# Kernel optimization log

Hardware: AMD Instinct MI355X
Metric: run time of the kernel (lower is better)

## Reference

```python
import jax, jax.numpy as jnp
import numpy as np

NUM_HEADS = 8
LN_EPS = 1e-5


def _pos_enc(h, w, dim, dtype):
    # PositionalEncodingPermute2D: channels = ceil(dim/2)
    ch = int(np.ceil(dim / 2))
    inv = jnp.asarray(1.0 / (10000.0 ** (np.arange(0, ch, 2, dtype=np.float32) / ch)))
    px = jnp.arange(h, dtype=jnp.float32)[:, None] * inv  # (h, ch//2)
    py = jnp.arange(w, dtype=jnp.float32)[:, None] * inv  # (w, ch//2)
    ex = jnp.concatenate([jnp.sin(px), jnp.cos(px)], -1)  # (h, ch)
    ey = jnp.concatenate([jnp.sin(py), jnp.cos(py)], -1)  # (w, ch)
    emb = jnp.concatenate([
        jnp.broadcast_to(ex[:, None, :], (h, w, ch)),
        jnp.broadcast_to(ey[None, :, :], (h, w, ch)),
    ], -1)[:, :, :dim]  # (h, w, dim)
    return emb.transpose(2, 0, 1).astype(dtype)  # (dim, h, w)


def _pool(x, s):
    # AdaptiveAvgPool2d(s) with h, w divisible by s
    b, c, h, w = x.shape
    return x.reshape(b, c, s, h // s, s, w // s).mean((3, 5))


def _dsc(y, dw_w, pw_w):
    # depthwise 3x3 (groups=C, pad 1, no bias) + pointwise 1x1 (no bias)
    dn = ('NCHW', 'OIHW', 'NCHW')
    y = jax.lax.conv_general_dilated(y, dw_w, (1, 1), 'SAME',
                                     feature_group_count=y.shape[1],
                                     dimension_numbers=dn)
    return jax.lax.conv_general_dilated(y, pw_w, (1, 1), 'SAME',
                                        dimension_numbers=dn)


def setup_inputs() -> dict:
    key = jax.random.key(0)
    ks = jax.random.split(key, 8)
    b, c, h, w = 8, 128, 128, 128
    s = 0.02
    return {
        'x': jax.random.normal(ks[0], (b, c, h, w), jnp.float32),
        'Wq': jax.random.normal(ks[1], (c, c), jnp.float32) * s,
        'Wkv': jax.random.normal(ks[2], (2 * c, c), jnp.float32) * s,
        'Wproj': jax.random.normal(ks[3], (c, c), jnp.float32) * s,
        'bproj': jnp.zeros((c,), jnp.float32),
        'dw_w': jax.random.normal(ks[4], (c, 1, 3, 3), jnp.float32) * np.sqrt(2.0 / 9.0),
        'pw_w': jax.random.normal(ks[5], (c, c, 1, 1), jnp.float32) * np.sqrt(2.0 / c),
        'ln_w': jnp.ones((c,), jnp.float32),
        'ln_b': jnp.zeros((c,), jnp.float32),
    }


def reference(x, Wq, Wkv, Wproj, bproj, dw_w, pw_w, ln_w, ln_b):
    b, c, h, w = x.shape
    m = NUM_HEADS
    hd = c // m
    scale = hd ** -0.5

    xp = x + _pos_enc(h, w, c, x.dtype)[None]        # (b,c,h,w)
    xt = xp.reshape(b, c, h * w).transpose(0, 2, 1)  # (b,hw,c)

    q = (xt @ Wq.T).reshape(b, h * w, m, hd).transpose(0, 2, 1, 3)  # (b,m,hw,hd)

    # four ASPP branches through the shared depthwise-separable conv
    branches = []
    for s in (8, 4, 2, 1):
        y = _dsc(_pool(xp, s), dw_w, pw_w)           # (b,c,s,s)
        branches.append(y.reshape(b, c, s * s).transpose(0, 2, 1))
    z = jnp.concatenate(branches, axis=1)            # (b,85,c)

    mu = z.mean(-1, keepdims=True)
    var = ((z - mu) ** 2).mean(-1, keepdims=True)
    z = (z - mu) / jnp.sqrt(var + LN_EPS) * ln_w + ln_b
    z = jax.nn.gelu(z, approximate=False)

    kvlen = z.shape[1]
    kv = (z @ Wkv.T).reshape(b, kvlen, 2, m, hd).transpose(2, 0, 3, 1, 4)  # (2,b,m,kv,hd)
    k, v = kv[0], kv[1]

    attn = jax.nn.softmax(jnp.einsum('bmqd,bmkd->bmqk', q, k) * scale, axis=-1)
    o = jnp.einsum('bmqk,bmkd->bmqd', attn, v)       # (b,m,hw,hd)
    o = o.transpose(0, 2, 1, 3).reshape(b, h * w, c)
    o = o @ Wproj.T + bproj                          # dropout p=0 (eval) is identity
    return o.transpose(0, 2, 1).reshape(b, c, h, w)
```

## Files before the change

### kernel.cpp

```cpp
#include <hip/hip_runtime.h>
#include <stdint.h>

#define OFF_EX   ((size_t)0)
#define OFF_EY   ((size_t)32768)
#define OFF_EXM  ((size_t)65536)
#define OFF_EYM  ((size_t)67584)
#define OFF_WQB  ((size_t)69632)
#define OFF_WPB  ((size_t)102400)
#define OFF_P8   ((size_t)135168)
#define OFF_KWS  ((size_t)393216)
#define OFF_VWS  ((size_t)589824)

typedef __attribute__((ext_vector_type(4)))  float f32x4;
typedef __attribute__((ext_vector_type(16))) float f32x16;
typedef __attribute__((ext_vector_type(8)))  short s16x8;
typedef __attribute__((ext_vector_type(4)))  unsigned int u32x4;

__device__ __forceinline__ uint16_t f2bf(float f){
  uint32_t u = __builtin_bit_cast(uint32_t, f);
  u += 0x7fffu + ((u >> 16) & 1u);
  return (uint16_t)(u >> 16);
}
__device__ __forceinline__ uint32_t cvtpk(float a, float b){
  uint32_t r;
  asm("v_cvt_pk_bf16_f32 %0, %1, %2" : "=v"(r) : "v"(a), "v"(b));
  return r;
}

__global__ __launch_bounds__(256) void kprep(const float* __restrict__ Wq,
                                             const float* __restrict__ Wproj,
                                             char* __restrict__ ws){
  int idx = blockIdx.x * 256 + threadIdx.x;
  float* EX = (float*)(ws + OFF_EX);
  float* EY = (float*)(ws + OFF_EY);
  float* EXM = (float*)(ws + OFF_EXM);
  float* EYM = (float*)(ws + OFF_EYM);
  uint16_t* WQB = (uint16_t*)(ws + OFF_WQB);
  uint16_t* WPB = (uint16_t*)(ws + OFF_WPB);
  if (idx < 8192){
    int i = idx >> 6, d = idx & 63;
    float inv = powf(10000.0f, -(float)(d & 31) * (1.0f/32.0f));
    float a = (float)i * inv;
    EX[idx] = (d < 32) ? sinf(a) : cosf(a);
  } else if (idx < 16384){
    int e = idx - 8192;
    int c = e >> 7, j = e & 127;
    float inv = powf(10000.0f, -(float)(c & 31) * (1.0f/32.0f));
    float a = (float)j * inv;
    EY[e] = (c < 32) ? sinf(a) : cosf(a);
  } else if (idx < 32768){
    int e = idx - 16384;
    WQB[e] = f2bf(Wq[e]);
  } else if (idx < 49152){
    int e = idx - 32768;
    WPB[e] = f2bf(Wproj[e]);
  } else if (idx < 49664){
    int e = idx - 49152; int r8 = e >> 6, c = e & 63;
    float inv = powf(10000.0f, -(float)(c & 31) * (1.0f/32.0f));
    float s = 0.f;
    for (int u = 0; u < 16; ++u){
      float a = (float)(r8*16 + u) * inv;
      s += (c < 32) ? sinf(a) : cosf(a);
    }
    EXM[e] = s * (1.0f/16.0f);
  } else if (idx < 50176){
    int e = idx - 49664; int c8 = e >> 6, c2 = e & 63;
    float inv = powf(10000.0f, -(float)(c2 & 31) * (1.0f/32.0f));
    float s = 0.f;
    for (int w = 0; w < 16; ++w){
      float a = (float)(c8*16 + w) * inv;
      s += (c2 < 32) ? sinf(a) : cosf(a);
    }
    EYM[e] = s * (1.0f/16.0f);
  }
}

__global__ __launch_bounds__(256) void kpool2(const float* __restrict__ x,
                                              char* __restrict__ ws){
  float* P8 = (float*)(ws + OFF_P8);
  int bx = blockIdx.x;
  int b = bx >> 7, c = bx & 127;
  int t = threadIdx.x, lane = t & 63, wv = t >> 6;
  const float* plane = x + ((size_t)(b*128 + c))*16384;
  float acc[8];
  #pragma unroll
  for (int r = 0; r < 8; ++r) acc[r] = 0.f;
  #pragma unroll
  for (int k = 0; k < 16; ++k){
    f32x4 v = *(const f32x4*)(plane + k*1024 + t*4);
    acc[k >> 1] += (v.x + v.y) + (v.z + v.w);
  }
  __shared__ float wred[4][64];
  int bc = (lane >> 2) & 7;
  #pragma unroll
  for (int br = 0; br < 8; ++br){
    float v = acc[br];
    v += __shfl_xor(v, 1);
    v += __shfl_xor(v, 2);
    v += __shfl_xor(v, 32);
    if ((lane & 3) == 0 && lane < 32) wred[wv][br*8 + bc] = v;
  }
  __syncthreads();
  if (t < 64){
    float s = wred[0][t] + wred[1][t] + wred[2][t] + wred[3][t];
    P8[((size_t)(b*128) + c)*64 + t] = s * (1.0f/256.0f);
  }
}

__global__ __launch_bounds__(256) void kaspp(const float* __restrict__ dww,
                                             const float* __restrict__ pww,
                                             const float* __restrict__ Wkv,
                                             const float* __restrict__ lnw,
                                             const float* __restrict__ lnb,
                                             char* __restrict__ ws){
  const float* P8  = (const float*)(ws + OFF_P8);
  const float* EXM = (const float*)(ws + OFF_EXM);
  const float* EYM = (const float*)(ws + OFF_EYM);
  uint16_t* KWS = (uint16_t*)(ws + OFF_KWS);
  uint16_t* VWS = (uint16_t*)(ws + OFF_VWS);
  int bx = blockIdx.x;
  int b = bx / 96;
  int pos = bx % 96;
  int t = threadIdx.x;

  if (pos >= 85){
    if (t < 128){
      int m = t >> 4, hd = t & 15;
      KWS[(((size_t)b*8 + m)*96 + pos)*16 + hd] = 0;
      VWS[(((size_t)b*8 + m)*16 + hd)*96 + pos] = 0;
    }
    return;
  }

  int s, si, sj;
  if (pos < 64){ s = 8; si = pos >> 3; sj = pos & 7; }
  else if (pos < 80){ int e = pos - 64; s = 4; si = e >> 2; sj = e & 3; }
  else if (pos < 84){ int e = pos - 80; s = 2; si = e >> 1; sj = e & 1; }
  else { s = 1; si = 0; sj = 0; }

  __shared__ float yl[128], zl[128], red[128], red2[128];

  float acc = 0.f;
  if (t < 128){
    int c = t;
    int bs = 8 / s;
    float y = 0.f;
    const float* p8 = P8 + ((size_t)(b*128) + c)*64;
    float binv = 1.0f / (float)(bs*bs);
    for (int di = -1; di <= 1; ++di)
      for (int dj = -1; dj <= 1; ++dj){
        int a = si + di, bb = sj + dj;
        if (a >= 0 && a < s && bb >= 0 && bb < s){
          float pv = 0.f;
          for (int u = 0; u < bs; ++u)
            for (int v = 0; v < bs; ++v){
              int r8 = a*bs + u, c8 = bb*bs + v;
              float pe = (c < 64) ? EXM[r8*64 + c] : EYM[c8*64 + (c - 64)];
              pv += p8[r8*8 + c8] + pe;
            }
          y += pv * binv * dww[c*9 + (di+1)*3 + (dj+1)];
        }
      }
    yl[t] = y;
  }
  __syncthreads();

  if (t < 128){
    const float* wr = pww + (size_t)t*128;
    for (int cin = 0; cin < 128; ++cin) acc += wr[cin] * yl[cin];
    red[t] = acc; red2[t] = acc*acc;
  }
  __syncthreads();
  for (int off = 64; off >= 1; off >>= 1){
    if (t < off){ red[t] += red[t+off]; red2[t] += red2[t+off]; }
    __syncthreads();
  }
  float mu  = red[0] * (1.0f/128.0f);
  float var = red2[0] * (1.0f/128.0f) - mu*mu;
  if (t < 128){
    float z = (acc - mu) * rsqrtf(var + 1e-5f) * lnw[t] + lnb[t];
    zl[t] = 0.5f * z * (1.0f + erff(z * 0.70710678118654752f));
  }
  __syncthreads();

  {
    float a2 = 0.f;
    const float* wr = Wkv + (size_t)t*128;
    for (int c2 = 0; c2 < 128; ++c2) a2 += wr[c2] * zl[c2];
    uint16_t bv = f2bf(a2);
    if (t < 128){
      int m = t >> 4, hd = t & 15;
      KWS[(((size_t)b*8 + m)*96 + pos)*16 + hd] = bv;
    } else {
      int tt = t - 128;
      int m = tt >> 4, hd = tt & 15;
      VWS[(((size_t)b*8 + m)*16 + hd)*96 + pos] = bv;
    }
  }
}

__global__ __launch_bounds__(256, 5) void kmain(const char* __restrict__ wsc,
                                                const float* __restrict__ x,
                                                const float* __restrict__ bproj,
                                                float* __restrict__ out){
  const char* ws = wsc;
  const uint16_t* WQB = (const uint16_t*)(ws + OFF_WQB);
  const uint16_t* WPB = (const uint16_t*)(ws + OFF_WPB);
  const uint16_t* KWS = (const uint16_t*)(ws + OFF_KWS);
  const uint16_t* VWS = (const uint16_t*)(ws + OFF_VWS);
  const float* EX = (const float*)(ws + OFF_EX);
  const float* EY = (const float*)(ws + OFF_EY);

  __shared__ __align__(16) char smem[32768];
  const int t = threadIdx.x;
  const int lane = t & 63;
  const int wv = t >> 6;
  const int bx = blockIdx.x;
  const int b = bx >> 8;
  const int pix0 = (bx & 255) * 64;
  const int i  = pix0 >> 7;
  const int j0 = pix0 & 127;

  #pragma unroll 1
  for (int half = 0; half < 2; ++half){
    {
      int csub = lane >> 4;
      int p4 = (lane & 15) * 4;
      #pragma unroll
      for (int it = 0; it < 4; ++it){
        int cl = wv*16 + it*4 + csub;
        int c = half*64 + cl;
        f32x4 v = *(const f32x4*)(x + ((size_t)(b*128 + c))*16384 + pix0 + p4);
        if (c < 64){
          float pe = EX[i*64 + c];
          v.x += pe; v.y += pe; v.z += pe; v.w += pe;
        } else {
          f32x4 pe = *(const f32x4*)(EY + (c - 64)*128 + j0 + p4);
          v.x += pe.x; v.y += pe.y; v.z += pe.z; v.w += pe.w;
        }
        *(f32x4*)(smem + 16384 + cl*256 + p4*4) = v;
      }
    }
    __syncthreads();
    {
      const float* tmp = (const float*)(smem + 16384);
      int pix = lane;
      float f[16];
      #pragma unroll
      for (int j = 0; j < 16; ++j) f[j] = tmp[(wv*16 + j)*64 + pix];
      uint32_t u[8];
      #pragma unroll
      for (int j = 0; j < 8; ++j) u[j] = cvtpk(f[2*j], f[2*j+1]);
      #pragma unroll
      for (int g = 0; g < 2; ++g){
        u32x4 w4 = { u[g*4+0], u[g*4+1], u[g*4+2], u[g*4+3] };
        int c0 = half*64 + wv*16 + g*8;
        *(u32x4*)(smem + pix*256 + ((c0*2) ^ ((pix & 7) << 4))) = w4;
      }
    }
    __syncthreads();
  }

  {
    int pixl = wv*16 + (lane & 15);
    s16x8 xfr[4];
    #pragma unroll
    for (int ks = 0; ks < 4; ++ks)
      xfr[ks] = *(const s16x8*)(smem + pixl*256 +
                 ((ks*64 + (lane >> 4)*16) ^ ((pixl & 7) << 4)));
    __syncthreads();
    #pragma unroll
    for (int nt = 0; nt < 8; ++nt){
      f32x4 acc = {0.f, 0.f, 0.f, 0.f};
      #pragma unroll
      for (int ks = 0; ks < 4; ++ks){
        s16x8 wfr = *(const s16x8*)(WQB + (nt*16 + (lane & 15))*128 + ks*32 + 8*(lane >> 4));
        acc = __builtin_amdgcn_mfma_f32_16x16x32_bf16(wfr, xfr[ks], acc, 0, 0, 0);
      }
      int nq0 = nt*16 + 4*(lane >> 4);
      uint32_t w0 = cvtpk(acc[0], acc[1]);
      uint32_t w1 = cvtpk(acc[2], acc[3]);
      *(uint32_t*)(smem + pixl*256 + ((nq0*2) ^ ((pixl & 7) << 4))) = w0;
      *(uint32_t*)(smem + pixl*256 + (((nq0 + 2)*2) ^ ((pixl & 7) << 4))) = w1;
    }
  }
  __syncthreads();

  {
    const int ph = wv & 1;
    const int h0 = (wv >> 1) * 4;
    const int hi = lane >> 5;
    const int pixq = ph*32 + (lane & 31);
    const float C1 = 0.36067376022224085f;

    #pragma unroll 1
    for (int h = h0; h < h0 + 4; ++h){
      const uint16_t* Kh = KWS + ((size_t)(b*8 + h))*1536;
      const uint16_t* Vh = VWS + ((size_t)(b*8 + h))*1536;
      s16x8 kf[3], vf[6];
      #pragma unroll
      for (int mt = 0; mt < 3; ++mt)
        kf[mt] = *(const s16x8*)(Kh + (mt*32 + (lane & 31))*16 + 8*hi);
      #pragma unroll
      for (int kc = 0; kc < 6; ++kc)
        vf[kc] = *(const s16x8*)(Vh + (lane & 15)*96 + kc*16 + 8*hi);
      s16x8 qf = *(const s16x8*)(smem + pixq*256 + ((h*32 + hi*16) ^ ((pixq & 7) << 4)));

      f32x16 zz;
      #pragma unroll
      for (int r = 0; r < 16; ++r) zz[r] = 0.f;
      f32x16 sa[3];
      #pragma unroll
      for (int mt = 0; mt < 3; ++mt)
        sa[mt] = __builtin_amdgcn_mfma_f32_32x32x16_bf16(kf[mt], qf, zz, 0, 0, 0);

      float mx = 0.f;
      #pragma unroll
      for (int r = 0; r < 16; ++r){
        mx = fmaxf(mx, sa[0][r]);
        mx = fmaxf(mx, sa[1][r]);
        mx = fmaxf(mx, sa[2][r]);
      }
      mx = fmaxf(mx, __shfl_xor(mx, 32));
      float sum = 0.f;
      #pragma unroll
      for (int r = 0; r < 16; ++r){
        float p0 = exp2f((sa[0][r] - mx)*C1); sa[0][r] = p0; sum += p0;
        float p1 = exp2f((sa[1][r] - mx)*C1); sa[1][r] = p1; sum += p1;
        int kvb = (r & 3) + 8*(r >> 2) + 4*hi;
        float p2 = (64 + kvb < 85) ? exp2f((sa[2][r] - mx)*C1) : 0.f;
        sa[2][r] = p2; sum += p2;
      }
      sum += __shfl_xor(sum, 32);
      float rinv = 1.0f / sum;

      f32x16 oacc = zz;
      #pragma unroll
      for (int mt = 0; mt < 3; ++mt){
        uint32_t u0[4], u1[4];
        #pragma unroll
        for (int q = 0; q < 4; ++q){
          u0[q] = cvtpk(sa[mt][4*q + 0], sa[mt][4*q + 1]);
          u1[q] = cvtpk(sa[mt][4*q + 2], sa[mt][4*q + 3]);
        }
        #pragma unroll
        for (int c2 = 0; c2 < 2; ++c2){
          uint32_t s0 = hi ? u0[2*c2] : u0[2*c2 + 1];
          uint32_t s1 = hi ? u1[2*c2] : u1[2*c2 + 1];
          uint32_t r0 = (uint32_t)__shfl_xor((int)s0, 32);
          uint32_t r1 = (uint32_t)__shfl_xor((int)s1, 32);
          u32x4 w4;
          w4.x = hi ? r0 : u0[2*c2];
          w4.y = hi ? r1 : u1[2*c2];
          w4.z = hi ? u0[2*c2 + 1] : r0;
          w4.w = hi ? u1[2*c2 + 1] : r1;
          oacc = __builtin_amdgcn_mfma_f32_32x32x16_bf16(
                   vf[mt*2 + c2], __builtin_bit_cast(s16x8, w4), oacc, 0, 0, 0);
        }
      }
      #pragma unroll
      for (int p = 0; p < 4; ++p){
        int hd0 = 4*hi + (p & 1)*2 + 8*(p >> 1);
        uint32_t uo = cvtpk(oacc[2*p]*rinv, oacc[2*p + 1]*rinv);
        int c0 = h*16 + hd0;
        *(uint32_t*)(smem + 16384 + pixq*256 + ((c0*2) ^ ((pixq & 7) << 4))) = uo;
      }
    }
  }
  __syncthreads();

  {
    int pixl = wv*16 + (lane & 15);
    s16x8 ofr[4];
    #pragma unroll
    for (int ks = 0; ks < 4; ++ks)
      ofr[ks] = *(const s16x8*)(smem + 16384 + pixl*256 +
                 ((ks*64 + (lane >> 4)*16) ^ ((pixl & 7) << 4)));
    int pixg = pix0 + pixl;
    float* outb = out + (size_t)b*128*16384 + pixg;
    #pragma unroll 2
    for (int mtc = 0; mtc < 8; ++mtc){
      f32x4 acc = {0.f, 0.f, 0.f, 0.f};
      #pragma unroll
      for (int ks = 0; ks < 4; ++ks){
        s16x8 wf = *(const s16x8*)(WPB + (mtc*16 + (lane & 15))*128 + ks*32 + 8*(lane >> 4));
        acc = __builtin_amdgcn_mfma_f32_16x16x32_bf16(wf, ofr[ks], acc, 0, 0, 0);
      }
      f32x4 bias = *(const f32x4*)(bproj + mtc*16 + 4*(lane >> 4));
      #pragma unroll
      for (int r = 0; r < 4; ++r){
        int cout = mtc*16 + 4*(lane >> 4) + r;
        outb[(size_t)cout*16384] = acc[r] + bias[r];
      }
    }
  }
}

extern "C" void kernel_launch(void* const* d_in, const int* in_sizes, int n_in,
                              void* d_out, int out_size, void* d_ws, size_t ws_size,
                              hipStream_t stream){
  const float* x     = (const float*)d_in[0];
  const float* Wq    = (const float*)d_in[1];
  const float* Wkv   = (const float*)d_in[2];
  const float* Wproj = (const float*)d_in[3];
  const float* bproj = (const float*)d_in[4];
  const float* dww   = (const float*)d_in[5];
  const float* pww   = (const float*)d_in[6];
  const float* lnw   = (const float*)d_in[7];
  const float* lnb   = (const float*)d_in[8];
  char* ws = (char*)d_ws;
  float* out = (float*)d_out;

  kprep<<<196, 256, 0, stream>>>(Wq, Wproj, ws);
  kpool2<<<1024, 256, 0, stream>>>(x, ws);
  kaspp<<<768, 256, 0, stream>>>(dww, pww, Wkv, lnw, lnb, ws);
  kmain<<<2048, 256, 0, stream>>>(ws, x, bproj, out);
}
```

Baseline: 243.7 us.

## Prefetch next head's K and Q fragments during attention loop, relax launch bounds

Restructures the per-head attention loop so the next head's K fragments and Q fragment are loaded while the current head's softmax and PV work runs. V loads move to after the QK MFMAs. The aim is to hide global/LDS load latency across iterations. It also drops the min-blocks-per-CU hint of 5, which lets the compiler use more registers for the extra live fragments but may lower occupancy.

```diff
diff --git a/kernel.cpp b/kernel.cpp
--- a/kernel.cpp
+++ b/kernel.cpp
@@ -199,10 +199,10 @@
   }
 }
 
-__global__ __launch_bounds__(256, 5) void kmain(const char* __restrict__ wsc,
-                                                const float* __restrict__ x,
-                                                const float* __restrict__ bproj,
-                                                float* __restrict__ out){
+__global__ __launch_bounds__(256) void kmain(const char* __restrict__ wsc,
+                                             const float* __restrict__ x,
+                                             const float* __restrict__ bproj,
+                                             float* __restrict__ out){
   const char* ws = wsc;
   const uint16_t* WQB = (const uint16_t*)(ws + OFF_WQB);
   const uint16_t* WPB = (const uint16_t*)(ws + OFF_WPB);
@@ -293,18 +293,18 @@
     const int pixq = ph*32 + (lane & 31);
     const float C1 = 0.36067376022224085f;
 
+    const uint16_t* Kb = KWS + (size_t)(b*8)*1536;
+    const uint16_t* Vb = VWS + (size_t)(b*8)*1536;
+
+    s16x8 kfc[3], qfc;
+    #pragma unroll
+    for (int mt = 0; mt < 3; ++mt)
+      kfc[mt] = *(const s16x8*)(Kb + (size_t)h0*1536 + (mt*32 + (lane & 31))*16 + 8*hi);
+    qfc = *(const s16x8*)(smem + pixq*256 + ((h0*32 + hi*16) ^ ((pixq & 7) << 4)));
+
     #pragma unroll 1
-    for (int h = h0; h < h0 + 4; ++h){
-      const uint16_t* Kh = KWS + ((size_t)(b*8 + h))*1536;
-      const uint16_t* Vh = VWS + ((size_t)(b*8 + h))*1536;
-      s16x8 kf[3], vf[6];
-      #pragma unroll
-      for (int mt = 0; mt < 3; ++mt)
-        kf[mt] = *(const s16x8*)(Kh + (mt*32 + (lane & 31))*16 + 8*hi);
-      #pragma unroll
-      for (int kc = 0; kc < 6; ++kc)
-        vf[kc] = *(const s16x8*)(Vh + (lane & 15)*96 + kc*16 + 8*hi);
-      s16x8 qf = *(const s16x8*)(smem + pixq*256 + ((h*32 + hi*16) ^ ((pixq & 7) << 4)));
+    for (int hh = 0; hh < 4; ++hh){
+      int h = h0 + hh;
 
       f32x16 zz;
       #pragma unroll
@@ -312,7 +312,19 @@
       f32x16 sa[3];
       #pragma unroll
       for (int mt = 0; mt < 3; ++mt)
-        sa[mt] = __builtin_amdgcn_mfma_f32_32x32x16_bf16(kf[mt], qf, zz, 0, 0, 0);
+        sa[mt] = __builtin_amdgcn_mfma_f32_32x32x16_bf16(kfc[mt], qfc, zz, 0, 0, 0);
+
+      s16x8 vf[6];
+      #pragma unroll
+      for (int kc = 0; kc < 6; ++kc)
+        vf[kc] = *(const s16x8*)(Vb + (size_t)h*1536 + (lane & 15)*96 + kc*16 + 8*hi);
+      s16x8 kfn[3], qfn;
+      if (hh < 3){
+        #pragma unroll
+        for (int mt = 0; mt < 3; ++mt)
+          kfn[mt] = *(const s16x8*)(Kb + (size_t)(h+1)*1536 + (mt*32 + (lane & 31))*16 + 8*hi);
+        qfn = *(const s16x8*)(smem + pixq*256 + (((h+1)*32 + hi*16) ^ ((pixq & 7) << 4)));
+      }
 
       float mx = 0.f;
       #pragma unroll
@@ -365,6 +377,12 @@
         int c0 = h*16 + hd0;
         *(uint32_t*)(smem + 16384 + pixq*256 + ((c0*2) ^ ((pixq & 7) << 4))) = uo;
       }
+
+      if (hh < 3){
+        #pragma unroll
+        for (int mt = 0; mt < 3; ++mt) kfc[mt] = kfn[mt];
+        qfc = qfn;
+      }
     }
   }
   __syncthreads();
```

After: 241.6 us. No clear change (-0.8%).
